# Performance work log

Hardware: AMD Instinct MI355X
Metric: run time of the kernel (lower is better)

Reference implementation:

```python
import jax, jax.numpy as jnp
import numpy as np

EPS = 1e-5
NEIGHBOR_K = 3
NEG_SLOPE = 0.2

def _conv(x, w):
    # x: [N,C,H,W], w: [O,I,3,3], stride 1, SAME padding
    return jax.lax.conv_general_dilated(
        x, w, window_strides=(1, 1), padding='SAME',
        dimension_numbers=('NCHW', 'OIHW', 'NCHW'))

def _bn(x, gamma, beta):
    # BatchNorm2d in training mode: batch statistics over (N,H,W), biased var
    m = x.mean(axis=(0, 2, 3), keepdims=True)
    v = x.var(axis=(0, 2, 3), keepdims=True)
    xn = (x - m) * jax.lax.rsqrt(v + EPS)
    return xn * gamma.reshape(1, -1, 1, 1) + beta.reshape(1, -1, 1, 1)

def _lrelu(x):
    return jnp.where(x >= 0, x, NEG_SLOPE * x)

def _maxpool2(x):
    return jax.lax.reduce_window(x, -jnp.inf, jax.lax.max,
                                 (1, 1, 2, 2), (1, 1, 2, 2), 'VALID')

def _features(x, w1, g1, b1, w2, g2, b2, w3, g3, b3, w4, g4, b4):
    x = _maxpool2(_lrelu(_bn(_conv(x, w1), g1, b1)))
    x = _maxpool2(_lrelu(_bn(_conv(x, w2), g2, b2)))
    x = _lrelu(_bn(_conv(x, w3), g3, b3))
    x = _lrelu(_bn(_conv(x, w4), g4, b4))
    return x  # [N, 64, 21, 21]

def setup_inputs() -> dict:
    key = jax.random.key(0)
    ks = jax.random.split(key, 8)
    inp = {
        'input1': jax.random.normal(ks[0], (32, 3, 84, 84), jnp.float32),
        'input2': jax.random.normal(ks[1], (5, 5, 3, 84, 84), jnp.float32),
        'w1': jax.random.normal(ks[2], (64, 3, 3, 3), jnp.float32) * 0.1,
        'g1': jax.random.uniform(ks[3], (64,), jnp.float32, 0.5, 1.5),
        'b1': jnp.zeros((64,), jnp.float32),
        'w2': jax.random.normal(ks[4], (64, 64, 3, 3), jnp.float32) * 0.1,
        'g2': jax.random.uniform(ks[5], (64,), jnp.float32, 0.5, 1.5),
        'b2': jnp.zeros((64,), jnp.float32),
        'w3': jax.random.normal(ks[6], (64, 64, 3, 3), jnp.float32) * 0.1,
        'g3': jax.random.uniform(ks[7], (64,), jnp.float32, 0.5, 1.5),
        'b3': jnp.zeros((64,), jnp.float32),
        'w4': jax.random.normal(jax.random.fold_in(key, 100), (64, 64, 3, 3), jnp.float32) * 0.1,
        'g4': jax.random.uniform(jax.random.fold_in(key, 101), (64,), jnp.float32, 0.5, 1.5),
        'b4': jnp.zeros((64,), jnp.float32),
    }
    return inp

def reference(input1, input2, w1, g1, b1, w2, g2, b2, w3, g3, b3, w4, g4, b4):
    params = (w1, g1, b1, w2, g2, b2, w3, g3, b3, w4, g4, b4)
    # Query features: [B, C, h, w]
    q = _features(input1, *params)
    B, C, h, w = q.shape
    hw = h * w
    Q = q.reshape(B, C, hw).transpose(0, 2, 1)            # [B, hw, C]
    qn = jnp.linalg.norm(Q, axis=2, keepdims=True)        # [B, hw, 1]
    # Support features, BN stats per class-batch (matches per-class forward)
    s = jax.vmap(lambda x: _features(x, *params))(input2) # [nc, shot, C, h, w]
    nc, shot = s.shape[0], s.shape[1]
    S = s.transpose(0, 2, 1, 3, 4).reshape(nc, C, shot * hw)  # [nc, C, M]
    sn = jnp.linalg.norm(S, axis=1, keepdims=True)            # [nc, 1, M]
    # Cosine similarities: [B, nc, hw, M]
    sims = jnp.einsum('bqc,ncm->bnqm', Q, S)
    sims = sims / (qn[:, None, :, :] * sn[None, :, :, :])
    topv = jax.lax.top_k(sims, NEIGHBOR_K)[0]              # [B, nc, hw, k]
    return topv.sum(axis=(2, 3))                           # [B, nc]
```

## Files before the change

### kernel.cpp

```cpp
#include <hip/hip_runtime.h>
#include <hip/hip_bf16.h>
#include <stdint.h>

#define NQ 32
#define NCLS 5
#define SHOT 5
#define NIMG 57
#define P1 7056
#define P2 1764
#define P3 441
#define PX 3528
#define MM (SHOT*P3)
#define EPSB 1e-5f
#define SLOPE 0.2f
#define NEGINF -3.4e38f
#define NREP 32
#define MSPAN 576
#define MRNG 4
#define QBLK 128
#define NQB 4
#define SLS 72

typedef __attribute__((ext_vector_type(8))) short short8;
typedef __attribute__((ext_vector_type(4))) float f32x4;

__device__ __forceinline__ unsigned short bf16bits(float v)
{
    __hip_bfloat16 h = __float2bfloat16(v);
    return *reinterpret_cast<unsigned short*>(&h);
}
__device__ __forceinline__ float bits2f(unsigned short u)
{
    unsigned int x = ((unsigned int)u) << 16;
    return *reinterpret_cast<float*>(&x);
}

__global__ void pack_all_k(const float* __restrict__ w1, const float* __restrict__ w2,
                           const float* __restrict__ w3, const float* __restrict__ w4,
                           unsigned short* __restrict__ wpk1, unsigned short* __restrict__ wpk2,
                           unsigned short* __restrict__ wpk3, unsigned short* __restrict__ wpk4,
                           float* __restrict__ sums)
{
    int i = blockIdx.x * 256 + threadIdx.x;
    if (i < 4 * 6 * 64 * 2 * NREP) sums[i] = 0.f;
    if (i < 3 * 36864) {
        int set = i / 36864, ii = i - set * 36864;
        const float* w = (set == 0) ? w2 : (set == 1) ? w3 : w4;
        unsigned short* wpk = (set == 0) ? wpk2 : (set == 1) ? wpk3 : wpk4;
        int j = ii & 7, lane = (ii >> 3) & 63, chunk = ii >> 9;
        int nt = chunk & 3, half = (chunk >> 2) & 1, t = chunk >> 3;
        int co = nt * 16 + (lane & 15);
        int ci = half * 32 + (lane >> 4) * 8 + j;
        wpk[ii] = bf16bits(w[co * 576 + ci * 9 + t]);
    } else {
        int ii = i - 3 * 36864;
        if (ii >= 4096) return;
        int j = ii & 7, lane = (ii >> 3) & 63, c8 = ii >> 9;
        int nt = c8 & 3, f = c8 >> 2;
        int co = nt * 16 + (lane & 15), q = lane >> 4;
        int k = q * 8 + j;
        float val = 0.f;
        if (f == 0) {
            int t = k >> 2, ci = k & 3;
            if (ci < 3) val = w1[co * 27 + ci * 9 + t];
        } else if (k < 4) {
            int ci = k & 3;
            if (ci < 3) val = w1[co * 27 + ci * 9 + 8];
        }
        wpk1[ii] = bf16bits(val);
    }
}

__global__ __launch_bounds__(256) void conv1m_k(const float* __restrict__ in1,
                                                const float* __restrict__ in2,
                                                const unsigned short* __restrict__ wpk1,
                                                __hip_bfloat16* __restrict__ xpool,
                                                float* __restrict__ sums)
{
    constexpr int S = 84, P = P1, MBLK = 256, NB = 28, SPAN = MBLK + 2 * S + 2;
    __shared__ __align__(16) unsigned short ls4[SPAN * 4];
    __shared__ float qs[4][64], qs2[4][64];
    int img = blockIdx.x / NB;
    int p0 = (blockIdx.x % NB) * MBLK;
    int tid = threadIdx.x, lane = tid & 63, wv = tid >> 6;
    int col = lane & 15, quad = lane >> 4;
    const float* in = (img < NQ) ? in1 + (size_t)img * 3 * P1
                                 : in2 + (size_t)(img - NQ) * 3 * P1;
    for (int u = tid; u < SPAN; u += 256) {
        int p = p0 - S - 1 + u;
        union { unsigned short us[4]; uint2 u2; } o;
        o.u2 = (uint2){0u, 0u};
        if (p >= 0 && p < P) {
            o.us[0] = bf16bits(in[p]);
            o.us[1] = bf16bits(in[P1 + p]);
            o.us[2] = bf16bits(in[2 * P1 + p]);
        }
        *(uint2*)(ls4 + u * 4) = o.u2;
    }
    const short8* wb = (const short8*)wpk1;
    short8 b0[4], b1[4];
    #pragma unroll
    for (int nt = 0; nt < 4; ++nt) {
        b0[nt] = wb[(size_t)(nt * 64 + lane)];
        b1[nt] = wb[(size_t)((4 + nt) * 64 + lane)];
    }
    int t0 = 2 * quad, t1 = t0 + 1;
    int d0 = (t0 / 3 - 1) * S + (t0 % 3 - 1);
    int d1 = (t1 / 3 - 1) * S + (t1 % 3 - 1);
    const int d8 = S + 1;
    int tx0 = t0 % 3, tx1 = t1 % 3;
    __syncthreads();
    f32x4 acc[4][4];
    #pragma unroll
    for (int mt = 0; mt < 4; ++mt)
        #pragma unroll
        for (int nt = 0; nt < 4; ++nt) acc[mt][nt] = (f32x4){0.f, 0.f, 0.f, 0.f};
    #pragma unroll
    for (int mt = 0; mt < 4; ++mt) {
        int pl = wv * 64 + mt * 16 + col;
        int xm = (p0 + pl) % S;
        int base = pl + S + 1;
        uint2 h0 = *(const uint2*)(ls4 + (base + d0) * 4);
        uint2 h1 = *(const uint2*)(ls4 + (base + d1) * 4);
        uint2 h8 = *(const uint2*)(ls4 + (base + d8) * 4);
        bool ok0 = (tx0 == 0) ? (xm >= 1) : ((tx0 == 2) ? (xm <= S - 2) : true);
        bool ok1 = (tx1 == 0) ? (xm >= 1) : ((tx1 == 2) ? (xm <= S - 2) : true);
        bool ok8 = (quad == 0) && (xm <= S - 2);
        if (!ok0) h0 = (uint2){0u, 0u};
        if (!ok1) h1 = (uint2){0u, 0u};
        if (!ok8) h8 = (uint2){0u, 0u};
        union { uint4 u; short8 s; } ca, cb;
        ca.u = (uint4){h0.x, h0.y, h1.x, h1.y};
        cb.u = (uint4){h8.x, h8.y, 0u, 0u};
        #pragma unroll
        for (int nt = 0; nt < 4; ++nt) {
            acc[mt][nt] = __builtin_amdgcn_mfma_f32_16x16x32_bf16(ca.s, b0[nt], acc[mt][nt], 0, 0, 0);
            acc[mt][nt] = __builtin_amdgcn_mfma_f32_16x16x32_bf16(cb.s, b1[nt], acc[mt][nt], 0, 0, 0);
        }
    }
    float s[4] = {0.f, 0.f, 0.f, 0.f}, s2[4] = {0.f, 0.f, 0.f, 0.f};
    __hip_bfloat16* ob = xpool + (size_t)img * PX * 64;
    #pragma unroll
    for (int mt = 0; mt < 4; ++mt) {
        int tb = p0 + wv * 64 + mt * 16 + quad * 4;
        #pragma unroll
        for (int reg = 0; reg < 4; ++reg) {
            int pr = tb + reg;
            if (pr < P) {
                #pragma unroll
                for (int nt = 0; nt < 4; ++nt) {
                    float v = acc[mt][nt][reg];
                    s[nt] += v;
                    s2[nt] = fmaf(v, v, s2[nt]);
                }
            }
        }
        #pragma unroll
        for (int pr2 = 0; pr2 < 2; ++pr2) {
            int m0 = tb + pr2 * 2;
            if (m0 < P) {
                #pragma unroll
                for (int nt = 0; nt < 4; ++nt) {
                    float v = fmaxf(acc[mt][nt][pr2 * 2], acc[mt][nt][pr2 * 2 + 1]);
                    ob[(size_t)(m0 >> 1) * 64 + nt * 16 + col] = __float2bfloat16(v);
                }
            }
        }
    }
    #pragma unroll
    for (int d = 16; d < 64; d <<= 1)
        #pragma unroll
        for (int nt = 0; nt < 4; ++nt) {
            s[nt] += __shfl_xor(s[nt], d, 64);
            s2[nt] += __shfl_xor(s2[nt], d, 64);
        }
    if (quad == 0) {
        #pragma unroll
        for (int nt = 0; nt < 4; ++nt) {
            qs[wv][nt * 16 + col] = s[nt];
            qs2[wv][nt * 16 + col] = s2[nt];
        }
    }
    __syncthreads();
    if (wv == 0) {
        int g = (img < NQ) ? 0 : 1 + (img - NQ) / SHOT;
        int rep = blockIdx.x & (NREP - 1);
        float ts = qs[0][lane] + qs[1][lane] + qs[2][lane] + qs[3][lane];
        float ts2 = qs2[0][lane] + qs2[1][lane] + qs2[2][lane] + qs2[3][lane];
        float* base = sums + ((size_t)(g * 64 + lane) * 2) * NREP + rep;
        atomicAdd(base, ts);
        atomicAdd(base + NREP, ts2);
    }
}

template <int S, int MBLK, int MODE, bool POOLX>
__global__ __launch_bounds__(256) void conv64m_k(const unsigned short* __restrict__ inv,
                                                 const unsigned short* __restrict__ wpk,
                                                 __hip_bfloat16* __restrict__ out,
                                                 float* __restrict__ sums,
                                                 const float* __restrict__ msin)
{
    constexpr int P = S * S;
    constexpr int MT = MBLK / 64;
    constexpr int NB = (P + MBLK - 1) / MBLK;
    constexpr int SPAN = MBLK + 2 * S + 2;
    __shared__ __align__(16) unsigned short ls[SPAN * 72];
    __shared__ float qs[4][64], qs2[4][64];
    int img = blockIdx.x / NB;
    int p0 = (blockIdx.x % NB) * MBLK;
    int tid = threadIdx.x;
    int lane = tid & 63, wv = tid >> 6;
    int col = lane & 15, quad = lane >> 4;
    int g = (img < NQ) ? 0 : 1 + (img - NQ) / SHOT;
    if constexpr (MODE == 0) {
        const unsigned short* ib = inv + (size_t)img * P * 64;
        for (int u = tid; u < SPAN * 8; u += 256) {
            int pix = u >> 3, part = u & 7;
            int p = p0 - S - 1 + pix;
            short8 v = {0, 0, 0, 0, 0, 0, 0, 0};
            if (p >= 0 && p < P) v = *(const short8*)(ib + (size_t)p * 64 + part * 8);
            *(short8*)(ls + pix * 72 + part * 8) = v;
        }
    } else {
        int part = tid & 7;
        float ba[8], bb[8];
        #pragma unroll
        for (int j = 0; j < 8; ++j) {
            float2 ab = ((const float2*)msin)[g * 64 + part * 8 + j];
            ba[j] = ab.x;
            bb[j] = ab.y;
        }
        if constexpr (MODE == 1) {
            const unsigned short* ib = inv + (size_t)img * P * 64;
            for (int u = tid; u < SPAN * 8; u += 256) {
                int pix = u >> 3;
                int p = p0 - S - 1 + pix;
                union { unsigned short us[8]; short8 s8; } o;
                #pragma unroll
                for (int j = 0; j < 8; ++j) o.us[j] = 0;
                if (p >= 0 && p < P) {
                    union { short8 s8; unsigned short us[8]; } x;
                    x.s8 = *(const short8*)(ib + (size_t)p * 64 + part * 8);
                    #pragma unroll
                    for (int j = 0; j < 8; ++j) {
                        float v = fmaf(bits2f(x.us[j]), ba[j], bb[j]);
                        v = fmaxf(v, SLOPE * v);
                        o.us[j] = bf16bits(v);
                    }
                }
                *(short8*)(ls + pix * 72 + part * 8) = o.s8;
            }
        } else {
            const unsigned short* ib2 = inv + (size_t)img * (2 * (size_t)P) * 64;
            for (int u = tid; u < SPAN * 8; u += 256) {
                int pix = u >> 3;
                int p = p0 - S - 1 + pix;
                union { unsigned short us[8]; short8 s8; } o;
                #pragma unroll
                for (int j = 0; j < 8; ++j) o.us[j] = 0;
                if (p >= 0 && p < P) {
                    int y = p / S, x = p - y * S;
                    const unsigned short* src = ib2 + ((size_t)(2 * y) * S + x) * 64 + part * 8;
                    union { short8 s8; unsigned short us[8]; } x0, x1;
                    x0.s8 = *(const short8*)src;
                    x1.s8 = *(const short8*)(src + (size_t)S * 64);
                    #pragma unroll
                    for (int j = 0; j < 8; ++j) {
                        float v = fmaxf(bits2f(x0.us[j]), bits2f(x1.us[j]));
                        v = fmaf(v, ba[j], bb[j]);
                        v = fmaxf(v, SLOPE * v);
                        o.us[j] = bf16bits(v);
                    }
                }
                *(short8*)(ls + pix * 72 + part * 8) = o.s8;
            }
        }
    }
    __syncthreads();
    f32x4 acc[MT][4];
    #pragma unroll
    for (int mt = 0; mt < MT; ++mt)
        #pragma unroll
        for (int nt = 0; nt < 4; ++nt) acc[mt][nt] = (f32x4){0.f, 0.f, 0.f, 0.f};
    bool mok0[MT], mok2[MT];
    #pragma unroll
    for (int mt = 0; mt < MT; ++mt) {
        int xm = (p0 + wv * (MT * 16) + mt * 16 + col) % S;
        mok0[mt] = xm >= 1;
        mok2[mt] = xm <= S - 2;
    }
    const short8* wb = (const short8*)wpk;
    #pragma unroll
    for (int ky = 0; ky < 3; ++ky) {
        #pragma unroll
        for (int kx = 0; kx < 3; ++kx) {
            int t = ky * 3 + kx;
            int d = (ky - 1) * S + (kx - 1);
            #pragma unroll
            for (int half = 0; half < 2; ++half) {
                short8 b[4];
                #pragma unroll
                for (int nt = 0; nt < 4; ++nt)
                    b[nt] = wb[((t * 2 + half) * 4 + nt) * 64 + lane];
                #pragma unroll
                for (int mt = 0; mt < MT; ++mt) {
                    int idx = wv * (MT * 16) + mt * 16 + col + S + 1 + d;
                    short8 a = *(const short8*)(ls + idx * 72 + half * 32 + quad * 8);
                    bool ok = (kx == 0) ? mok0[mt] : (kx == 2) ? mok2[mt] : true;
                    if (!ok) a = (short8){0, 0, 0, 0, 0, 0, 0, 0};
                    #pragma unroll
                    for (int nt = 0; nt < 4; ++nt)
                        acc[mt][nt] = __builtin_amdgcn_mfma_f32_16x16x32_bf16(a, b[nt], acc[mt][nt], 0, 0, 0);
                }
            }
        }
    }
    float s[4] = {0.f, 0.f, 0.f, 0.f}, s2[4] = {0.f, 0.f, 0.f, 0.f};
    __hip_bfloat16* ob = out + (size_t)img * (POOLX ? P / 2 : P) * 64;
    #pragma unroll
    for (int mt = 0; mt < MT; ++mt) {
        int tb = p0 + wv * (MT * 16) + mt * 16 + quad * 4;
        #pragma unroll
        for (int reg = 0; reg < 4; ++reg) {
            int pr = tb + reg;
            if (pr < P) {
                #pragma unroll
                for (int nt = 0; nt < 4; ++nt) {
                    float v = acc[mt][nt][reg];
                    s[nt] += v;
                    s2[nt] = fmaf(v, v, s2[nt]);
                }
            }
        }
        if constexpr (POOLX) {
            #pragma unroll
            for (int pr2 = 0; pr2 < 2; ++pr2) {
                int m0 = tb + pr2 * 2;
                if (m0 < P) {
                    #pragma unroll
                    for (int nt = 0; nt < 4; ++nt) {
                        float v = fmaxf(acc[mt][nt][pr2 * 2], acc[mt][nt][pr2 * 2 + 1]);
                        ob[(size_t)(m0 >> 1) * 64 + nt * 16 + col] = __float2bfloat16(v);
                    }
                }
            }
        } else {
            #pragma unroll
            for (int reg = 0; reg < 4; ++reg) {
                int pr = tb + reg;
                if (pr < P) {
                    #pragma unroll
                    for (int nt = 0; nt < 4; ++nt)
                        ob[(size_t)pr * 64 + nt * 16 + col] = __float2bfloat16(acc[mt][nt][reg]);
                }
            }
        }
    }
    #pragma unroll
    for (int d = 16; d < 64; d <<= 1)
        #pragma unroll
        for (int nt = 0; nt < 4; ++nt) {
            s[nt] += __shfl_xor(s[nt], d, 64);
            s2[nt] += __shfl_xor(s2[nt], d, 64);
        }
    if (quad == 0) {
        #pragma unroll
        for (int nt = 0; nt < 4; ++nt) {
            qs[wv][nt * 16 + col] = s[nt];
            qs2[wv][nt * 16 + col] = s2[nt];
        }
    }
    __syncthreads();
    if (wv == 0) {
        int rep = blockIdx.x & (NREP - 1);
        float ts = qs[0][lane] + qs[1][lane] + qs[2][lane] + qs[3][lane];
        float ts2 = qs2[0][lane] + qs2[1][lane] + qs2[2][lane] + qs2[3][lane];
        float* base = sums + ((size_t)(g * 64 + lane) * 2) * NREP + rep;
        atomicAdd(base, ts);
        atomicAdd(base + NREP, ts2);
    }
}

__global__ void finalize_k(const float* __restrict__ sums, float* __restrict__ ms,
                           const float* __restrict__ gamma, const float* __restrict__ beta, int P)
{
    int i = blockIdx.x * blockDim.x + threadIdx.x;
    if (i >= 6 * 64) return;
    int g = i >> 6, c = i & 63;
    const float* ps = sums + (size_t)i * 2 * NREP;
    float s = 0.f, s2 = 0.f;
    #pragma unroll
    for (int r = 0; r < NREP; ++r) { s += ps[r]; s2 += ps[NREP + r]; }
    float cnt = (float)((g == 0 ? NQ : SHOT) * P);
    float mean = s / cnt;
    float var = s2 / cnt - mean * mean;
    float a = rsqrtf(var + EPSB) * gamma[c];
    ms[i * 2] = a;
    ms[i * 2 + 1] = fmaf(-mean, a, beta[c]);
}

__global__ __launch_bounds__(256) void bnnorm_k(const unsigned short* __restrict__ x,
                                                const float* __restrict__ ms,
                                                __hip_bfloat16* __restrict__ out)
{
    int lane = threadIdx.x & 63, wvr = threadIdx.x >> 6;
    int pix = blockIdx.x * 4 + wvr;
    if (pix >= NIMG * P3) return;
    int img = pix / P3;
    int g = (img < NQ) ? 0 : 1 + (img - NQ) / SHOT;
    float v = fmaf(bits2f(x[(size_t)pix * 64 + lane]), ms[(g * 64 + lane) * 2], ms[(g * 64 + lane) * 2 + 1]);
    v = v >= 0.f ? v : SLOPE * v;
    float ss = v * v;
    #pragma unroll
    for (int d = 32; d > 0; d >>= 1) ss += __shfl_xor(ss, d, 64);
    out[(size_t)pix * 64 + lane] = __float2bfloat16(v * rsqrtf(ss));
}

__device__ __forceinline__ void ins3(float v, float& t0, float& t1, float& t2)
{
    t2 = __builtin_amdgcn_fmed3f(v, t1, t2);
    t1 = __builtin_amdgcn_fmed3f(v, t0, t1);
    t0 = fmaxf(t0, v);
}

template <int PAT>
__device__ __forceinline__ void swzmerge(float& t0, float& t1, float& t2)
{
    float u0 = __int_as_float(__builtin_amdgcn_ds_swizzle(__float_as_int(t0), PAT));
    float u1 = __int_as_float(__builtin_amdgcn_ds_swizzle(__float_as_int(t1), PAT));
    float u2 = __int_as_float(__builtin_amdgcn_ds_swizzle(__float_as_int(t2), PAT));
    ins3(u0, t0, t1, t2);
    ins3(u1, t0, t1, t2);
    ins3(u2, t0, t1, t2);
}

__global__ __launch_bounds__(256, 5) void sim_part_k(const __hip_bfloat16* __restrict__ fhat,
                                                     float* __restrict__ part)
{
    __shared__ __align__(16) unsigned short sl[64 * SLS];
    int t = blockIdx.x;
    int mr = t & 3;
    int qb = (t >> 2) & 3;
    int n = (t >> 4) % NCLS;
    int bq = t / (16 * NCLS);
    int tid = threadIdx.x, lane = tid & 63, wv = tid >> 6;
    int col = lane & 15, quad = lane >> 4;
    short8 a0[2], a1[2];
    #pragma unroll
    for (int g = 0; g < 2; ++g) {
        int q = qb * QBLK + wv * 32 + g * 16 + col;
        int qc = q < P3 ? q : P3 - 1;
        const unsigned short* qp = (const unsigned short*)fhat + ((size_t)bq * P3 + qc) * 64;
        a0[g] = *(const short8*)(qp + quad * 8);
        a1[g] = *(const short8*)(qp + 32 + quad * 8);
    }
    const unsigned short* sp = (const unsigned short*)fhat + (size_t)(NQ + n * SHOT) * P3 * 64;
    int m_lo = mr * MSPAN;
    int m_cnt = MM - m_lo; if (m_cnt > MSPAN) m_cnt = MSPAN;
    int nch = (m_cnt + 63) >> 6;
    float t0[2][4], t1[2][4], t2[2][4];
    #pragma unroll
    for (int g = 0; g < 2; ++g)
        #pragma unroll
        for (int r = 0; r < 4; ++r) { t0[g][r] = NEGINF; t1[g][r] = NEGINF; t2[g][r] = NEGINF; }
    int srow = tid >> 3, scc = (tid & 7) * 8;
    const unsigned short* gp = sp + (size_t)(m_lo + srow) * 64 + scc;
    unsigned short* ld0 = sl + srow * SLS + scc;
    const unsigned short* sr = sl + col * SLS + quad * 8;
    int mcur = m_lo + srow;
    const short8 z8 = {0, 0, 0, 0, 0, 0, 0, 0};
    short8 v0 = z8, v1 = z8;
    if (mcur < MM) v0 = *(const short8*)gp;
    if (mcur + 32 < MM) v1 = *(const short8*)(gp + 32 * 64);
    for (int c = 0; c < nch; ++c) {
        __syncthreads();
        *(short8*)ld0 = v0;
        *(short8*)(ld0 + 32 * SLS) = v1;
        __syncthreads();
        if (c + 1 < nch) {
            gp += 64 * 64;
            mcur += 64;
            v0 = z8; v1 = z8;
            if (mcur < MM) v0 = *(const short8*)gp;
            if (mcur + 32 < MM) v1 = *(const short8*)(gp + 32 * 64);
        }
        int m0 = m_lo + c * 64;
        #pragma unroll
        for (int mt = 0; mt < 4; ++mt) {
            if (m0 + mt * 16 < MM) {
                short8 b0 = *(const short8*)(sr + mt * (16 * SLS));
                short8 b1 = *(const short8*)(sr + mt * (16 * SLS) + 32);
                #pragma unroll
                for (int g = 0; g < 2; ++g) {
                    f32x4 acc = {0.f, 0.f, 0.f, 0.f};
                    acc = __builtin_amdgcn_mfma_f32_16x16x32_bf16(a0[g], b0, acc, 0, 0, 0);
                    acc = __builtin_amdgcn_mfma_f32_16x16x32_bf16(a1[g], b1, acc, 0, 0, 0);
                    #pragma unroll
                    for (int r = 0; r < 4; ++r) ins3(acc[r], t0[g][r], t1[g][r], t2[g][r]);
                }
            }
        }
    }
    #pragma unroll
    for (int g = 0; g < 2; ++g)
        #pragma unroll
        for (int r = 0; r < 4; ++r) {
            swzmerge<0x041F>(t0[g][r], t1[g][r], t2[g][r]);
            swzmerge<0x081F>(t0[g][r], t1[g][r], t2[g][r]);
            swzmerge<0x101F>(t0[g][r], t1[g][r], t2[g][r]);
            swzmerge<0x201F>(t0[g][r], t1[g][r], t2[g][r]);
        }
    if (col == 0) {
        #pragma unroll
        for (int g = 0; g < 2; ++g)
            #pragma unroll
            for (int r = 0; r < 4; ++r) {
                int ql = wv * 32 + g * 16 + quad * 4 + r;
                float* pp = part + ((((size_t)(bq * NCLS + n) * NQB + qb) * MRNG + mr) * QBLK + ql) * 3;
                pp[0] = t0[g][r];
                pp[1] = t1[g][r];
                pp[2] = t2[g][r];
            }
    }
}

__global__ __launch_bounds__(256) void sim_merge_k(const float* __restrict__ part,
                                                   float* __restrict__ out)
{
    __shared__ float red[4];
    int b = blockIdx.x;
    int tid = threadIdx.x, lane = tid & 63, wv = tid >> 6;
    float s = 0.f;
    for (int q = tid; q < P3; q += 256) {
        int qb = q >> 7, ql = q & 127;
        const float* pp = part + (((size_t)b * NQB + qb) * MRNG * QBLK + ql) * 3;
        float v0 = pp[0], v1 = pp[1], v2 = pp[2];
        #pragma unroll
        for (int mr = 1; mr < 4; ++mr) {
            const float* pm = pp + (size_t)mr * (QBLK * 3);
            ins3(pm[0], v0, v1, v2);
            ins3(pm[1], v0, v1, v2);
            ins3(pm[2], v0, v1, v2);
        }
        s += v0 + v1 + v2;
    }
    #pragma unroll
    for (int d = 32; d > 0; d >>= 1) s += __shfl_xor(s, d, 64);
    if (lane == 0) red[wv] = s;
    __syncthreads();
    if (tid == 0) out[b] = red[0] + red[1] + red[2] + red[3];
}

extern "C" void kernel_launch(void* const* d_in, const int* in_sizes, int n_in,
                              void* d_out, int out_size, void* d_ws, size_t ws_size,
                              hipStream_t stream)
{
    const float* input1 = (const float*)d_in[0];
    const float* input2 = (const float*)d_in[1];
    const float* w1 = (const float*)d_in[2];
    const float* g1 = (const float*)d_in[3];
    const float* b1 = (const float*)d_in[4];
    const float* w2 = (const float*)d_in[5];
    const float* g2 = (const float*)d_in[6];
    const float* b2 = (const float*)d_in[7];
    const float* w3 = (const float*)d_in[8];
    const float* g3 = (const float*)d_in[9];
    const float* b3 = (const float*)d_in[10];
    const float* w4 = (const float*)d_in[11];
    const float* g4 = (const float*)d_in[12];
    const float* b4 = (const float*)d_in[13];
    float* out = (float*)d_out;

    char* w8 = (char*)d_ws;
    const size_t oB = 51480576;
    const size_t oT = oB + 12870144;
    const size_t STG = 6 * 64 * 2 * NREP * sizeof(float);
    __hip_bfloat16* xpool1 = (__hip_bfloat16*)(w8 + 0);
    __hip_bfloat16* conv3raw = (__hip_bfloat16*)(w8 + 0);
    __hip_bfloat16* conv4raw = (__hip_bfloat16*)(w8 + 9652608);
    __hip_bfloat16* fhat = (__hip_bfloat16*)(w8 + 16087680);
    __hip_bfloat16* xpool2 = (__hip_bfloat16*)(w8 + oB);
    float* sums = (float*)(w8 + oT);
    float* ms = (float*)(w8 + oT + 4 * STG);
    unsigned short* wpk2 = (unsigned short*)(w8 + oT + 4 * STG + 12288);
    unsigned short* wpk3 = (unsigned short*)(w8 + oT + 4 * STG + 12288 + 73728);
    unsigned short* wpk4 = (unsigned short*)(w8 + oT + 4 * STG + 12288 + 147456);
    unsigned short* wpk1 = (unsigned short*)(w8 + oT + 4 * STG + 12288 + 221184);
    const size_t oP = oT + 4 * STG + 12288 + 221184 + 8192;
    float* part = (float*)(w8 + oP);
    if (ws_size < oP + (size_t)NQ * NCLS * NQB * MRNG * QBLK * 3 * sizeof(float)) return;
    float* sums1 = sums;
    float* sums2 = sums + 6 * 64 * 2 * NREP;
    float* sums3 = sums2 + 6 * 64 * 2 * NREP;
    float* sums4 = sums3 + 6 * 64 * 2 * NREP;

    pack_all_k<<<448, 256, 0, stream>>>(w1, w2, w3, w4, wpk1, wpk2, wpk3, wpk4, sums);

    conv1m_k<<<NIMG * 28, 256, 0, stream>>>(input1, input2, wpk1, xpool1, sums1);
    finalize_k<<<2, 256, 0, stream>>>(sums1, ms + 0, g1, b1, P1);
    conv64m_k<42, 256, 2, true><<<NIMG * 7, 256, 0, stream>>>(
        (const unsigned short*)xpool1, wpk2, xpool2, sums2, ms + 0);
    finalize_k<<<2, 256, 0, stream>>>(sums2, ms + 768, g2, b2, P2);
    conv64m_k<21, 128, 2, false><<<NIMG * 4, 256, 0, stream>>>(
        (const unsigned short*)xpool2, wpk3, conv3raw, sums3, ms + 768);
    finalize_k<<<2, 256, 0, stream>>>(sums3, ms + 1536, g3, b3, P3);
    conv64m_k<21, 128, 1, false><<<NIMG * 4, 256, 0, stream>>>(
        (const unsigned short*)conv3raw, wpk4, conv4raw, sums4, ms + 1536);
    finalize_k<<<2, 256, 0, stream>>>(sums4, ms + 2304, g4, b4, P3);
    bnnorm_k<<<6285, 256, 0, stream>>>((const unsigned short*)conv4raw, ms + 2304, fhat);
    sim_part_k<<<NQ * NCLS * NQB * MRNG, 256, 0, stream>>>(fhat, part);
    sim_merge_k<<<NQ * NCLS, 256, 0, stream>>>(part, out);
}
```

Before: 224.2 us.

## Load support tiles directly from global and double query rows per block

The similarity kernel drops the shared-memory staging of support features and the two barriers per chunk. Each wave now loads its MFMA B fragments straight from global memory, relying on cache hits. The query block grows from 128 to 256 rows (four 16-row groups per wave), so each support fragment is reused across more MFMAs, and grid size halves. The merge kernel indexing is updated to match. The trade-off is more redundant global/L2 traffic across waves, higher register pressure (occupancy hint lowered to 4), and masking for the partial last tile.

```diff
diff --git a/kernel.cpp b/kernel.cpp
--- a/kernel.cpp
+++ b/kernel.cpp
@@ -17,9 +17,9 @@
 #define NREP 32
 #define MSPAN 576
 #define MRNG 4
-#define QBLK 128
-#define NQB 4
-#define SLS 72
+#define QBLK 256
+#define NQB 2
+#define QG 4
 
 typedef __attribute__((ext_vector_type(8))) short short8;
 typedef __attribute__((ext_vector_type(4))) float f32x4;
@@ -434,21 +434,20 @@
     ins3(u2, t0, t1, t2);
 }
 
-__global__ __launch_bounds__(256, 5) void sim_part_k(const __hip_bfloat16* __restrict__ fhat,
+__global__ __launch_bounds__(256, 4) void sim_part_k(const __hip_bfloat16* __restrict__ fhat,
                                                      float* __restrict__ part)
 {
-    __shared__ __align__(16) unsigned short sl[64 * SLS];
     int t = blockIdx.x;
     int mr = t & 3;
-    int qb = (t >> 2) & 3;
-    int n = (t >> 4) % NCLS;
-    int bq = t / (16 * NCLS);
+    int qb = (t >> 2) & 1;
+    int n = (t >> 3) % NCLS;
+    int bq = t / (8 * NCLS);
     int tid = threadIdx.x, lane = tid & 63, wv = tid >> 6;
     int col = lane & 15, quad = lane >> 4;
-    short8 a0[2], a1[2];
-    #pragma unroll
-    for (int g = 0; g < 2; ++g) {
-        int q = qb * QBLK + wv * 32 + g * 16 + col;
+    short8 a0[QG], a1[QG];
+    #pragma unroll
+    for (int g = 0; g < QG; ++g) {
+        int q = qb * QBLK + wv * (QG * 16) + g * 16 + col;
         int qc = q < P3 ? q : P3 - 1;
         const unsigned short* qp = (const unsigned short*)fhat + ((size_t)bq * P3 + qc) * 64;
         a0[g] = *(const short8*)(qp + quad * 8);
@@ -457,52 +456,43 @@
     const unsigned short* sp = (const unsigned short*)fhat + (size_t)(NQ + n * SHOT) * P3 * 64;
     int m_lo = mr * MSPAN;
     int m_cnt = MM - m_lo; if (m_cnt > MSPAN) m_cnt = MSPAN;
-    int nch = (m_cnt + 63) >> 6;
-    float t0[2][4], t1[2][4], t2[2][4];
-    #pragma unroll
-    for (int g = 0; g < 2; ++g)
+    int ntiles = (m_cnt + 15) >> 4;
+    float t0[QG][4], t1[QG][4], t2[QG][4];
+    #pragma unroll
+    for (int g = 0; g < QG; ++g)
         #pragma unroll
         for (int r = 0; r < 4; ++r) { t0[g][r] = NEGINF; t1[g][r] = NEGINF; t2[g][r] = NEGINF; }
-    int srow = tid >> 3, scc = (tid & 7) * 8;
-    const unsigned short* gp = sp + (size_t)(m_lo + srow) * 64 + scc;
-    unsigned short* ld0 = sl + srow * SLS + scc;
-    const unsigned short* sr = sl + col * SLS + quad * 8;
-    int mcur = m_lo + srow;
-    const short8 z8 = {0, 0, 0, 0, 0, 0, 0, 0};
-    short8 v0 = z8, v1 = z8;
-    if (mcur < MM) v0 = *(const short8*)gp;
-    if (mcur + 32 < MM) v1 = *(const short8*)(gp + 32 * 64);
-    for (int c = 0; c < nch; ++c) {
-        __syncthreads();
-        *(short8*)ld0 = v0;
-        *(short8*)(ld0 + 32 * SLS) = v1;
-        __syncthreads();
-        if (c + 1 < nch) {
-            gp += 64 * 64;
-            mcur += 64;
-            v0 = z8; v1 = z8;
-            if (mcur < MM) v0 = *(const short8*)gp;
-            if (mcur + 32 < MM) v1 = *(const short8*)(gp + 32 * 64);
-        }
-        int m0 = m_lo + c * 64;
-        #pragma unroll
-        for (int mt = 0; mt < 4; ++mt) {
-            if (m0 + mt * 16 < MM) {
-                short8 b0 = *(const short8*)(sr + mt * (16 * SLS));
-                short8 b1 = *(const short8*)(sr + mt * (16 * SLS) + 32);
-                #pragma unroll
-                for (int g = 0; g < 2; ++g) {
-                    f32x4 acc = {0.f, 0.f, 0.f, 0.f};
-                    acc = __builtin_amdgcn_mfma_f32_16x16x32_bf16(a0[g], b0, acc, 0, 0, 0);
-                    acc = __builtin_amdgcn_mfma_f32_16x16x32_bf16(a1[g], b1, acc, 0, 0, 0);
-                    #pragma unroll
-                    for (int r = 0; r < 4; ++r) ins3(acc[r], t0[g][r], t1[g][r], t2[g][r]);
-                }
-            }
-        }
-    }
-    #pragma unroll
-    for (int g = 0; g < 2; ++g)
+    const unsigned short* bpt = sp + ((size_t)m_lo + col) * 64 + quad * 8;
+    #pragma unroll 4
+    for (int ti = 0; ti < ntiles; ++ti) {
+        short8 b0 = *(const short8*)bpt;
+        short8 b1 = *(const short8*)(bpt + 32);
+        bpt += 16 * 64;
+        int mrow = m_lo + ti * 16;
+        if (mrow + 16 <= MM) {
+            #pragma unroll
+            for (int g = 0; g < QG; ++g) {
+                f32x4 acc = {0.f, 0.f, 0.f, 0.f};
+                acc = __builtin_amdgcn_mfma_f32_16x16x32_bf16(a0[g], b0, acc, 0, 0, 0);
+                acc = __builtin_amdgcn_mfma_f32_16x16x32_bf16(a1[g], b1, acc, 0, 0, 0);
+                #pragma unroll
+                for (int r = 0; r < 4; ++r) ins3(acc[r], t0[g][r], t1[g][r], t2[g][r]);
+            }
+        } else {
+            bool valid = (mrow + col) < MM;
+            #pragma unroll
+            for (int g = 0; g < QG; ++g) {
+                f32x4 acc = {0.f, 0.f, 0.f, 0.f};
+                acc = __builtin_amdgcn_mfma_f32_16x16x32_bf16(a0[g], b0, acc, 0, 0, 0);
+                acc = __builtin_amdgcn_mfma_f32_16x16x32_bf16(a1[g], b1, acc, 0, 0, 0);
+                #pragma unroll
+                for (int r = 0; r < 4; ++r)
+                    ins3(valid ? acc[r] : NEGINF, t0[g][r], t1[g][r], t2[g][r]);
+            }
+        }
+    }
+    #pragma unroll
+    for (int g = 0; g < QG; ++g)
         #pragma unroll
         for (int r = 0; r < 4; ++r) {
             swzmerge<0x041F>(t0[g][r], t1[g][r], t2[g][r]);
@@ -512,10 +502,10 @@
         }
     if (col == 0) {
         #pragma unroll
-        for (int g = 0; g < 2; ++g)
+        for (int g = 0; g < QG; ++g)
             #pragma unroll
             for (int r = 0; r < 4; ++r) {
-                int ql = wv * 32 + g * 16 + quad * 4 + r;
+                int ql = wv * (QG * 16) + g * 16 + quad * 4 + r;
                 float* pp = part + ((((size_t)(bq * NCLS + n) * NQB + qb) * MRNG + mr) * QBLK + ql) * 3;
                 pp[0] = t0[g][r];
                 pp[1] = t1[g][r];
@@ -532,7 +522,7 @@
     int tid = threadIdx.x, lane = tid & 63, wv = tid >> 6;
     float s = 0.f;
     for (int q = tid; q < P3; q += 256) {
-        int qb = q >> 7, ql = q & 127;
+        int qb = q >> 8, ql = q & 255;
         const float* pp = part + (((size_t)b * NQB + qb) * MRNG * QBLK + ql) * 3;
         float v0 = pp[0], v1 = pp[1], v2 = pp[2];
         #pragma unroll
```

Result: slower. 386.5 us (+72.4%).
